# Performance work log

Hardware: AMD Instinct MI355X
Metric: run time of the kernel (lower is better)

The kernel has to match this reference:

```python
import jax, jax.numpy as jnp
import numpy as np

N_NODES = 50000
N_EDGES = 800000
N_GRAPHS = 512
HIDDEN = 256
NODE_FEAT = 9
LAYERS = 4


def setup_inputs() -> dict:
    key = jax.random.key(0)
    ks = jax.random.split(key, 9)
    x = jax.random.normal(ks[0], (N_NODES, NODE_FEAT), dtype=jnp.float32)
    edge_index = jax.random.randint(ks[1], (2, N_EDGES), 0, N_NODES, dtype=jnp.int64)
    batch = jnp.sort(jax.random.randint(ks[2], (N_NODES,), 0, N_GRAPHS, dtype=jnp.int64))
    embed_W = jax.random.normal(ks[3], (NODE_FEAT, HIDDEN), dtype=jnp.float32) * (1.0 / np.sqrt(NODE_FEAT))
    embed_b = jnp.zeros((HIDDEN,), dtype=jnp.float32)
    conv_W = jax.random.normal(ks[4], (LAYERS, HIDDEN, HIDDEN), dtype=jnp.float32) * (1.0 / np.sqrt(HIDDEN))
    conv_b = jnp.zeros((LAYERS, HIDDEN), dtype=jnp.float32)
    out_W = jax.random.normal(ks[5], (HIDDEN, 1), dtype=jnp.float32) * (1.0 / np.sqrt(HIDDEN))
    out_b = jnp.zeros((1,), dtype=jnp.float32)
    return {"x": x, "edge_index": edge_index, "batch": batch,
            "embed_W": embed_W, "embed_b": embed_b,
            "conv_W": conv_W, "conv_b": conv_b,
            "out_W": out_W, "out_b": out_b}


def reference(x, edge_index, batch, embed_W, embed_b, conv_W, conv_b, out_W, out_b):
    n = x.shape[0]
    src, dst = edge_index[0], edge_index[1]
    # GCN symmetric normalization with self-loops: deg includes the self-loop (+1)
    deg = jax.ops.segment_sum(jnp.ones(src.shape[0], x.dtype), dst, num_segments=n) + 1.0
    dinv = jax.lax.rsqrt(deg)                       # [N]
    norm_e = dinv[src] * dinv[dst]                  # [E] edge coefficient
    self_coef = (dinv * dinv)[:, None]              # [N,1] self-loop coefficient

    h = jax.nn.relu(x @ embed_W + embed_b)          # [N,H]
    for l in range(conv_W.shape[0]):
        hw = h @ conv_W[l]                          # [N,H] transform first
        msg = hw[src] * norm_e[:, None]             # [E,H] gather + scale
        agg = jax.ops.segment_sum(msg, dst, num_segments=n)  # scatter-add
        agg = agg + hw * self_coef                  # self-loop contribution
        h = jax.nn.relu(agg + conv_b[l])

    # global mean pool over graph ids
    sums = jax.ops.segment_sum(h, batch, num_segments=N_GRAPHS)           # [G,H]
    cnt = jax.ops.segment_sum(jnp.ones(n, h.dtype), batch, num_segments=N_GRAPHS)
    pooled = sums / jnp.maximum(cnt, 1.0)[:, None]
    return pooled @ out_W + out_b                   # [G,1]
```

## Files before the change

### kernel.cpp

```cpp
#include <hip/hip_runtime.h>

#define N_NODES 50000
#define N_EDGES 800000
#define N_GRAPHS 512
#define HIDDEN 256
#define NODE_FEAT 9
#define LAYERS 4
#define SCAN_BS 256
#define SCAN_NB ((N_NODES + SCAN_BS - 1) / SCAN_BS)

typedef float floatx4 __attribute__((ext_vector_type(4)));
typedef short short8 __attribute__((ext_vector_type(8)));

__device__ __forceinline__ float bf2f(unsigned u) {
    unsigned v = u << 16;
    float f;
    __builtin_memcpy(&f, &v, 4);
    return f;
}
__device__ __forceinline__ unsigned short f2bf(float f) {
    unsigned v;
    __builtin_memcpy(&v, &f, 4);
    v += 0x7FFFu + ((v >> 16) & 1u);
    return (unsigned short)(v >> 16);
}

__global__ void count_kernel(const int* __restrict__ dst, int* __restrict__ cnt, int E) {
    int e = blockIdx.x * blockDim.x + threadIdx.x;
    if (e < E) atomicAdd(&cnt[dst[e]], 1);
}

__global__ __launch_bounds__(SCAN_BS) void bsum_kernel(const int* __restrict__ cnt, int* __restrict__ bsum, int N) {
    __shared__ int sdata[SCAN_BS];
    int t = threadIdx.x;
    int i = blockIdx.x * SCAN_BS + t;
    sdata[t] = (i < N) ? cnt[i] : 0;
    __syncthreads();
    #pragma unroll
    for (int off = SCAN_BS / 2; off > 0; off >>= 1) {
        if (t < off) sdata[t] += sdata[t + off];
        __syncthreads();
    }
    if (t == 0) bsum[blockIdx.x] = sdata[0];
}

__global__ __launch_bounds__(SCAN_BS) void bscan_kernel(const int* __restrict__ bsum, int* __restrict__ boff) {
    __shared__ int sdata[SCAN_BS];
    int t = threadIdx.x;
    int v = (t < SCAN_NB) ? bsum[t] : 0;
    sdata[t] = v;
    __syncthreads();
    #pragma unroll
    for (int off = 1; off < SCAN_BS; off <<= 1) {
        int u = (t >= off) ? sdata[t - off] : 0;
        __syncthreads();
        sdata[t] += u;
        __syncthreads();
    }
    if (t < SCAN_NB) boff[t] = sdata[t] - v;
}

__global__ __launch_bounds__(SCAN_BS) void rowfill_kernel(int* __restrict__ cnt,
                                                          const int* __restrict__ boff,
                                                          int* __restrict__ row_ptr,
                                                          float* __restrict__ dinv, int N, int E) {
    __shared__ int sdata[SCAN_BS];
    int t = threadIdx.x;
    int i = blockIdx.x * SCAN_BS + t;
    int c = (i < N) ? cnt[i] : 0;
    sdata[t] = c;
    __syncthreads();
    #pragma unroll
    for (int off = 1; off < SCAN_BS; off <<= 1) {
        int u = (t >= off) ? sdata[t - off] : 0;
        __syncthreads();
        sdata[t] += u;
        __syncthreads();
    }
    if (i < N) {
        int pos = boff[blockIdx.x] + sdata[t] - c;
        row_ptr[i] = pos;
        cnt[i] = pos;
        dinv[i] = rsqrtf((float)(c + 1));
    }
    if (i == N) row_ptr[N] = E;
}

__global__ void fill_kernel(const int* __restrict__ src, const int* __restrict__ dst,
                            int* __restrict__ cursor, int* __restrict__ col_src, int E) {
    int e = blockIdx.x * blockDim.x + threadIdx.x;
    if (e < E) {
        int pos = atomicAdd(&cursor[dst[e]], 1);
        col_src[pos] = src[e];
    }
}

__global__ void findstart_kernel(const int* __restrict__ batch, int* __restrict__ gstart) {
    int g = blockIdx.x * blockDim.x + threadIdx.x;
    if (g > N_GRAPHS) return;
    if (g == N_GRAPHS) { gstart[g] = N_NODES; return; }
    int lo = 0, hi = N_NODES;
    while (lo < hi) {
        int mid = (lo + hi) >> 1;
        if (batch[mid] < g) lo = mid + 1; else hi = mid;
    }
    gstart[g] = lo;
}

__global__ __launch_bounds__(256) void packW_kernel(const float* __restrict__ W,
                                                    unsigned short* __restrict__ Wsw) {
    int idx = blockIdx.x * 256 + threadIdx.x;
    int lane = idx & 63;
    int ct   = (idx >> 6) & 15;
    int ks   = (idx >> 10) & 7;
    int l    = idx >> 13;
    int n = ct * 16 + (lane & 15);
    int kbase = ks * 32 + (lane >> 4) * 8;
    const float* Wl = W + (size_t)l * HIDDEN * HIDDEN;
    alignas(16) unsigned short tmp[8];
    #pragma unroll
    for (int j = 0; j < 8; j++)
        tmp[j] = f2bf(Wl[(size_t)(kbase + j) * HIDDEN + n]);
    *(uint4*)&Wsw[(size_t)idx * 8] = *(const uint4*)tmp;
}

__global__ __launch_bounds__(256) void embed_kernel(const float* __restrict__ x,
                                                    const float* __restrict__ W,
                                                    const float* __restrict__ b,
                                                    unsigned short* __restrict__ h) {
    int n = blockIdx.x;
    int c = threadIdx.x;
    float acc = b[c];
    #pragma unroll
    for (int k = 0; k < NODE_FEAT; k++)
        acc += x[n * NODE_FEAT + k] * W[k * HIDDEN + c];
    h[(size_t)n * HIDDEN + c] = f2bf(fmaxf(acc, 0.0f));
}

__global__ __launch_bounds__(256) void gemm_mfma(const unsigned short* __restrict__ hin,
                                                 const unsigned short* __restrict__ Wsw,
                                                 unsigned short* __restrict__ hwout, int N) {
    __shared__ unsigned short As[64][264];
    int t = threadIdx.x;
    int n0 = blockIdx.x * 64;
    const uint4* h4 = (const uint4*)hin;
    #pragma unroll
    for (int i = 0; i < 8; i++) {
        int j = t + i * 256;
        int r = j >> 5;
        int c = j & 31;
        int n = n0 + r;
        uint4 v = make_uint4(0u, 0u, 0u, 0u);
        if (n < N) v = h4[(size_t)n * 32 + c];
        *(uint4*)&As[r][c * 8] = v;
    }
    __syncthreads();

    int wv = t >> 6, lane = t & 63, quad = lane >> 4, l15 = lane & 15;
    floatx4 acc[4][4];
    #pragma unroll
    for (int i = 0; i < 4; i++)
        #pragma unroll
        for (int j = 0; j < 4; j++)
            acc[i][j] = (floatx4){0.f, 0.f, 0.f, 0.f};

    const short8* Wl = (const short8*)Wsw;
    #pragma unroll
    for (int ks = 0; ks < 8; ks++) {
        short8 a[4], b[4];
        #pragma unroll
        for (int rt = 0; rt < 4; rt++)
            a[rt] = *(const short8*)&As[rt * 16 + l15][ks * 32 + quad * 8];
        #pragma unroll
        for (int ci = 0; ci < 4; ci++)
            b[ci] = Wl[(size_t)(ks * 16 + wv * 4 + ci) * 64 + lane];
        #pragma unroll
        for (int rt = 0; rt < 4; rt++)
            #pragma unroll
            for (int ci = 0; ci < 4; ci++)
                acc[rt][ci] = __builtin_amdgcn_mfma_f32_16x16x32_bf16(a[rt], b[ci], acc[rt][ci], 0, 0, 0);
    }

    #pragma unroll
    for (int rt = 0; rt < 4; rt++) {
        #pragma unroll
        for (int ci = 0; ci < 4; ci++) {
            int col = (wv * 4 + ci) * 16 + l15;
            int rowb = n0 + rt * 16 + quad * 4;
            #pragma unroll
            for (int reg = 0; reg < 4; reg++) {
                int rr = rowb + reg;
                if (rr < N) hwout[(size_t)rr * HIDDEN + col] = f2bf(acc[rt][ci][reg]);
            }
        }
    }
}

__global__ __launch_bounds__(128) void agg_kernel(const unsigned short* __restrict__ hw,
                                                  const int* __restrict__ row_ptr,
                                                  const int* __restrict__ col_src,
                                                  const float* __restrict__ dinv,
                                                  const float* __restrict__ bias,
                                                  unsigned short* __restrict__ hout) {
    __shared__ int sidx[128];
    __shared__ float snrm[128];
    int n = blockIdx.x;
    int t = threadIdx.x;
    float dn = dinv[n];
    int e0 = row_ptr[n], e1 = row_ptr[n + 1];
    unsigned su = *(const unsigned*)&hw[(size_t)n * HIDDEN + 2 * t];
    float selfc = dn * dn;
    float ax = bf2f(su & 0xFFFFu) * selfc + bias[2 * t];
    float ay = bf2f(su >> 16)     * selfc + bias[2 * t + 1];
    for (int cs = e0; cs < e1; cs += 128) {
        int cnt = e1 - cs; if (cnt > 128) cnt = 128;
        __syncthreads();
        if (t < cnt) {
            int s = col_src[cs + t];
            sidx[t] = s;
            snrm[t] = dinv[s] * dn;
        }
        __syncthreads();
        for (int i = 0; i < cnt; i++) {
            float nr = snrm[i];
            unsigned u = *(const unsigned*)&hw[(size_t)sidx[i] * HIDDEN + 2 * t];
            ax += nr * bf2f(u & 0xFFFFu);
            ay += nr * bf2f(u >> 16);
        }
    }
    unsigned packed = (unsigned)f2bf(fmaxf(ax, 0.0f)) | ((unsigned)f2bf(fmaxf(ay, 0.0f)) << 16);
    *(unsigned*)&hout[(size_t)n * HIDDEN + 2 * t] = packed;
}

__global__ __launch_bounds__(256) void pool2_kernel(const unsigned short* __restrict__ h,
                                                    const int* __restrict__ gstart,
                                                    const float* __restrict__ outW,
                                                    const float* __restrict__ outb,
                                                    float* __restrict__ out) {
    __shared__ float sred[4];
    int g = blockIdx.x;
    int t = threadIdx.x;
    int s = gstart[g], e = gstart[g + 1];
    int half = t >> 7;
    int tc = t & 127;
    float w0 = outW[2 * tc], w1 = outW[2 * tc + 1];
    float acc = 0.0f;
    for (int n = s + half; n < e; n += 2) {
        unsigned u = *(const unsigned*)&h[(size_t)n * HIDDEN + 2 * tc];
        acc += w0 * bf2f(u & 0xFFFFu) + w1 * bf2f(u >> 16);
    }
    #pragma unroll
    for (int off = 32; off > 0; off >>= 1) acc += __shfl_down(acc, off, 64);
    if ((t & 63) == 0) sred[t >> 6] = acc;
    __syncthreads();
    if (t == 0) {
        float tot = sred[0] + sred[1] + sred[2] + sred[3];
        float cnt = (float)(e - s);
        out[g] = tot / fmaxf(cnt, 1.0f) + outb[0];
    }
}

extern "C" void kernel_launch(void* const* d_in, const int* in_sizes, int n_in,
                              void* d_out, int out_size, void* d_ws, size_t ws_size,
                              hipStream_t stream) {
    const float* x     = (const float*)d_in[0];
    const int*   edge  = (const int*)d_in[1];
    const int*   src   = edge;
    const int*   dst   = edge + N_EDGES;
    const int*   batch = (const int*)d_in[2];
    const float* embW  = (const float*)d_in[3];
    const float* embb  = (const float*)d_in[4];
    const float* convW = (const float*)d_in[5];
    const float* convb = (const float*)d_in[6];
    const float* outW  = (const float*)d_in[7];
    const float* outb  = (const float*)d_in[8];
    float* out = (float*)d_out;

    char* ws = (char*)d_ws;
    size_t off = 0;
    auto take = [&](size_t bytes) { char* p = ws + off; off += (bytes + 255) & ~(size_t)255; return p; };
    int*   cnt     = (int*)  take((size_t)N_NODES * 4);
    int*   row_ptr = (int*)  take((size_t)(N_NODES + 1) * 4);
    int*   col_src = (int*)  take((size_t)N_EDGES * 4);
    float* dinv    = (float*)take((size_t)N_NODES * 4);
    int*   bsum    = (int*)  take((size_t)SCAN_NB * 4);
    int*   boff    = (int*)  take((size_t)SCAN_NB * 4);
    int*   gstart  = (int*)  take((size_t)(N_GRAPHS + 1) * 4);
    unsigned short* Wsw = (unsigned short*)take((size_t)LAYERS * 8 * 16 * 64 * 8 * 2);
    unsigned short* h0  = (unsigned short*)take((size_t)N_NODES * HIDDEN * 2);
    unsigned short* h1  = (unsigned short*)take((size_t)N_NODES * HIDDEN * 2);

    hipMemsetAsync(cnt, 0, (size_t)N_NODES * 4, stream);

    count_kernel<<<(N_EDGES + 255) / 256, 256, 0, stream>>>(dst, cnt, N_EDGES);
    bsum_kernel<<<SCAN_NB, SCAN_BS, 0, stream>>>(cnt, bsum, N_NODES);
    bscan_kernel<<<1, SCAN_BS, 0, stream>>>(bsum, boff);
    rowfill_kernel<<<SCAN_NB + 1, SCAN_BS, 0, stream>>>(cnt, boff, row_ptr, dinv, N_NODES, N_EDGES);
    fill_kernel<<<(N_EDGES + 255) / 256, 256, 0, stream>>>(src, dst, cnt, col_src, N_EDGES);
    findstart_kernel<<<3, 256, 0, stream>>>(batch, gstart);

    packW_kernel<<<128, 256, 0, stream>>>(convW, Wsw);
    embed_kernel<<<N_NODES, 256, 0, stream>>>(x, embW, embb, h0);

    unsigned short* ha = h0;
    unsigned short* hb = h1;
    for (int l = 0; l < LAYERS; l++) {
        gemm_mfma<<<(N_NODES + 63) / 64, 256, 0, stream>>>(ha, Wsw + (size_t)l * 65536, hb, N_NODES);
        agg_kernel<<<N_NODES, 128, 0, stream>>>(hb, row_ptr, col_src, dinv, convb + (size_t)l * HIDDEN, ha);
    }

    pool2_kernel<<<N_GRAPHS, 256, 0, stream>>>(ha, gstart, outW, outb, out);
}
```

Before: 537.5 us.

## Stage GEMM output through LDS and use one wavefront per node in aggregation

The GEMM epilogue now writes bf16 results into the shared A tile and then stores full rows with coalesced 16-byte writes, replacing scattered 2-byte global stores. The aggregation kernel assigns one 64-lane wavefront per node, four nodes per block. Each lane handles four features with 8-byte loads, and edge index/norm pairs are staged in per-wave shared memory without block-wide barriers. This cuts block-launch overhead and sync cost and widens the memory accesses. It relies on wave-synchronous behaviour for the shared edge buffer and leaves an unused leftover load.

```diff
diff --git a/kernel.cpp b/kernel.cpp
--- a/kernel.cpp
+++ b/kernel.cpp
@@ -181,55 +181,76 @@
                 acc[rt][ci] = __builtin_amdgcn_mfma_f32_16x16x32_bf16(a[rt], b[ci], acc[rt][ci], 0, 0, 0);
     }
 
+    __syncthreads();
     #pragma unroll
     for (int rt = 0; rt < 4; rt++) {
         #pragma unroll
         for (int ci = 0; ci < 4; ci++) {
             int col = (wv * 4 + ci) * 16 + l15;
-            int rowb = n0 + rt * 16 + quad * 4;
+            int rowb = rt * 16 + quad * 4;
             #pragma unroll
-            for (int reg = 0; reg < 4; reg++) {
-                int rr = rowb + reg;
-                if (rr < N) hwout[(size_t)rr * HIDDEN + col] = f2bf(acc[rt][ci][reg]);
-            }
+            for (int reg = 0; reg < 4; reg++)
+                As[rowb + reg][col] = f2bf(acc[rt][ci][reg]);
         }
     }
-}
-
-__global__ __launch_bounds__(128) void agg_kernel(const unsigned short* __restrict__ hw,
+    __syncthreads();
+    #pragma unroll
+    for (int i = 0; i < 8; i++) {
+        int j = t + i * 256;
+        int r = j >> 5;
+        int c = j & 31;
+        int n = n0 + r;
+        if (n < N)
+            *(uint4*)&hwout[(size_t)n * HIDDEN + c * 8] = *(const uint4*)&As[r][c * 8];
+    }
+}
+
+__global__ __launch_bounds__(256) void agg_kernel(const unsigned short* __restrict__ hw,
                                                   const int* __restrict__ row_ptr,
                                                   const int* __restrict__ col_src,
                                                   const float* __restrict__ dinv,
                                                   const float* __restrict__ bias,
                                                   unsigned short* __restrict__ hout) {
-    __shared__ int sidx[128];
-    __shared__ float snrm[128];
-    int n = blockIdx.x;
-    int t = threadIdx.x;
+    __shared__ uint2 sEdge[4][64];
+    int wv = threadIdx.x >> 6, lane = threadIdx.x & 63;
+    int n = blockIdx.x * 4 + wv;
+    if (n >= N_NODES) return;
     float dn = dinv[n];
     int e0 = row_ptr[n], e1 = row_ptr[n + 1];
-    unsigned su = *(const unsigned*)&hw[(size_t)n * HIDDEN + 2 * t];
+
+    uint2 su = *(const uint2*)(hw + (size_t)n * HIDDEN) + make_uint2(0,0), s2;
+    s2 = ((const uint2*)(hw + (size_t)n * HIDDEN))[lane];
+    float4 b4 = *(const float4*)&bias[4 * lane];
     float selfc = dn * dn;
-    float ax = bf2f(su & 0xFFFFu) * selfc + bias[2 * t];
-    float ay = bf2f(su >> 16)     * selfc + bias[2 * t + 1];
-    for (int cs = e0; cs < e1; cs += 128) {
-        int cnt = e1 - cs; if (cnt > 128) cnt = 128;
-        __syncthreads();
-        if (t < cnt) {
-            int s = col_src[cs + t];
-            sidx[t] = s;
-            snrm[t] = dinv[s] * dn;
+    float a0 = bf2f(s2.x & 0xFFFFu) * selfc + b4.x;
+    float a1 = bf2f(s2.x >> 16)     * selfc + b4.y;
+    float a2 = bf2f(s2.y & 0xFFFFu) * selfc + b4.z;
+    float a3 = bf2f(s2.y >> 16)     * selfc + b4.w;
+    (void)su;
+
+    for (int cs = e0; cs < e1; cs += 64) {
+        int cnt = e1 - cs; if (cnt > 64) cnt = 64;
+        if (lane < cnt) {
+            int s = col_src[cs + lane];
+            float nr = dinv[s] * dn;
+            unsigned nrb;
+            __builtin_memcpy(&nrb, &nr, 4);
+            sEdge[wv][lane] = make_uint2((unsigned)s, nrb);
         }
-        __syncthreads();
         for (int i = 0; i < cnt; i++) {
-            float nr = snrm[i];
-            unsigned u = *(const unsigned*)&hw[(size_t)sidx[i] * HIDDEN + 2 * t];
-            ax += nr * bf2f(u & 0xFFFFu);
-            ay += nr * bf2f(u >> 16);
+            uint2 p = sEdge[wv][i];
+            float nr;
+            __builtin_memcpy(&nr, &p.y, 4);
+            uint2 u = ((const uint2*)(hw + (size_t)p.x * HIDDEN))[lane];
+            a0 += nr * bf2f(u.x & 0xFFFFu);
+            a1 += nr * bf2f(u.x >> 16);
+            a2 += nr * bf2f(u.y & 0xFFFFu);
+            a3 += nr * bf2f(u.y >> 16);
         }
     }
-    unsigned packed = (unsigned)f2bf(fmaxf(ax, 0.0f)) | ((unsigned)f2bf(fmaxf(ay, 0.0f)) << 16);
-    *(unsigned*)&hout[(size_t)n * HIDDEN + 2 * t] = packed;
+    unsigned p0 = (unsigned)f2bf(fmaxf(a0, 0.0f)) | ((unsigned)f2bf(fmaxf(a1, 0.0f)) << 16);
+    unsigned p1 = (unsigned)f2bf(fmaxf(a2, 0.0f)) | ((unsigned)f2bf(fmaxf(a3, 0.0f)) << 16);
+    ((uint2*)(hout + (size_t)n * HIDDEN))[lane] = make_uint2(p0, p1);
 }
 
 __global__ __launch_bounds__(256) void pool2_kernel(const unsigned short* __restrict__ h,
@@ -306,7 +327,7 @@
     unsigned short* hb = h1;
     for (int l = 0; l < LAYERS; l++) {
         gemm_mfma<<<(N_NODES + 63) / 64, 256, 0, stream>>>(ha, Wsw + (size_t)l * 65536, hb, N_NODES);
-        agg_kernel<<<N_NODES, 128, 0, stream>>>(hb, row_ptr, col_src, dinv, convb + (size_t)l * HIDDEN, ha);
+        agg_kernel<<<(N_NODES + 3) / 4, 256, 0, stream>>>(hb, row_ptr, col_src, dinv, convb + (size_t)l * HIDDEN, ha);
     }
 
     pool2_kernel<<<N_GRAPHS, 256, 0, stream>>>(ha, gstart, outW, outb, out);
```

New measurement: 532.6 us. No clear change (-0.9%).
